# Performance work log

Measured on AMD Instinct MI355X. Metric: run time of the kernel, lower is better.

The kernel has to match this reference:

```python
import jax, jax.numpy as jnp
import numpy as np


def setup_inputs() -> dict:
    key = jax.random.key(0)
    k1, k2 = jax.random.split(key)
    pred = jax.random.normal(k1, (4, 8192, 3), dtype=jnp.float32)
    target = jax.random.normal(k2, (4, 8192, 3), dtype=jnp.float32)
    return {"pred": pred, "target": target}


def reference(pred, target):
    # Pairwise squared distances via the expansion ||p-q||^2 = ||p||^2 + ||q||^2 - 2 p.q
    # Avoids materializing the O(B*M*N*3) diff tensor of the naive broadcast.
    p_sq = jnp.sum(pred * pred, axis=-1)          # [B, M]
    q_sq = jnp.sum(target * target, axis=-1)      # [B, N]
    cross = jnp.einsum("bmd,bnd->bmn", pred, target)  # [B, M, N]
    dist_sq = p_sq[:, :, None] + q_sq[:, None, :] - 2.0 * cross  # [B, M, N]
    min_dist_pred = jnp.min(dist_sq, axis=2).mean(axis=1)    # [B] min over target per pred point
    min_dist_target = jnp.min(dist_sq, axis=1).mean(axis=1)  # [B] min over pred per target point
    return jnp.mean(min_dist_pred + min_dist_target)
```

## Files before the change

kernel.cpp:

```cpp
#include <hip/hip_runtime.h>


#define THREADS 256
#define P 8
#define S 16
#define G 128
#define TILE 128
#define LSTRIDE (TILE + 1)

__global__ __launch_bounds__(THREADS) void chamfer_min_kernel(
    const float* __restrict__ pred, const float* __restrict__ target,
    float* __restrict__ out, int M, float scale) {
  const int blocksPerDir = M / G;
  int pblk = blockIdx.x % blocksPerDir;
  int bd = blockIdx.x / blocksPerDir;
  int dir = bd & 1;
  int b = bd >> 1;
  const float* src = (dir ? target : pred) + (size_t)b * M * 3;
  const float* ref = (dir ? pred : target) + (size_t)b * M * 3;

  __shared__ float4 lds[S * LSTRIDE];

  int t = threadIdx.x;
  int g = t >> 4;
  int l = t & 15;

  float cm[P], ax[P], ay[P], az[P];
  int pbase = pblk * G;
#pragma unroll
  for (int j = 0; j < P; ++j) {
    int pt = pbase + l + 16 * j;
    float x = src[pt * 3 + 0], y = src[pt * 3 + 1], z = src[pt * 3 + 2];
    cm[j] = x * x + y * y + z * z;
    ax[j] = -2.f * x;
    ay[j] = -2.f * y;
    az[j] = -2.f * z;
  }
  float mins[P];
#pragma unroll
  for (int j = 0; j < P; ++j) mins[j] = 3.0e38f;

  const int sliceLen = M / S;
  const int ntiles = sliceLen / TILE;
  for (int k = 0; k < ntiles; ++k) {
    __syncthreads();
#pragma unroll
    for (int i = 0; i < (S * TILE) / THREADS; ++i) {
      int idx = t + THREADS * i;
      int s = idx >> 7;
      int jj = idx & (TILE - 1);
      int n = s * sliceLen + k * TILE + jj;
      float qx = ref[n * 3 + 0], qy = ref[n * 3 + 1], qz = ref[n * 3 + 2];
      lds[s * LSTRIDE + jj] = make_float4(qx, qy, qz, qx * qx + qy * qy + qz * qz);
    }
    __syncthreads();
    const float4* tp = lds + g * LSTRIDE;
#pragma unroll 2
    for (int j = 0; j < TILE; j += 4) {
      float4 q0 = tp[j + 0];
      float4 q1 = tp[j + 1];
      float4 q2 = tp[j + 2];
      float4 q3 = tp[j + 3];
#pragma unroll
      for (int p = 0; p < P; ++p) {
        float d0 = fmaf(ax[p], q0.x, fmaf(ay[p], q0.y, fmaf(az[p], q0.z, q0.w)));
        float d1 = fmaf(ax[p], q1.x, fmaf(ay[p], q1.y, fmaf(az[p], q1.z, q1.w)));
        float d2 = fmaf(ax[p], q2.x, fmaf(ay[p], q2.y, fmaf(az[p], q2.z, q2.w)));
        float d3 = fmaf(ax[p], q3.x, fmaf(ay[p], q3.y, fmaf(az[p], q3.z, q3.w)));
        mins[p] = fminf(fminf(mins[p], d0), d1);
        mins[p] = fminf(fminf(mins[p], d2), d3);
      }
    }
  }

  __syncthreads();
  float* lmin = (float*)lds;
  float* lcm = (float*)lds + S * G;
#pragma unroll
  for (int j = 0; j < P; ++j) {
    lmin[g * G + (l + 16 * j)] = mins[j];
    if (g == 0) lcm[l + 16 * j] = cm[j];
  }
  __syncthreads();
  float v = 0.f;
  if (t < G) {
    float mn = 3.0e38f;
#pragma unroll
    for (int s = 0; s < S; ++s) mn = fminf(mn, lmin[s * G + t]);
    v = lcm[t] + mn;
  }
  for (int off = 32; off > 0; off >>= 1) v += __shfl_down(v, off, 64);
  __shared__ float ws[THREADS / 64];
  if ((t & 63) == 0) ws[t >> 6] = v;
  __syncthreads();
  if (t == 0) {
    float bsum = 0.f;
#pragma unroll
    for (int w = 0; w < THREADS / 64; ++w) bsum += ws[w];
    atomicAdd(out, bsum * scale);
  }
}

extern "C" void kernel_launch(void* const* d_in, const int* in_sizes, int n_in,
                              void* d_out, int out_size, void* d_ws,
                              size_t ws_size, hipStream_t stream) {
  const float* pred = (const float*)d_in[0];
  const float* target = (const float*)d_in[1];
  float* out = (float*)d_out;
  const int B = 4;
  const int M = in_sizes[0] / (B * 3);

  float scale = 1.0f / (float)(B * M);

  hipMemsetAsync(out, 0, sizeof(float), stream);
  int blocks = B * 2 * (M / G);
  chamfer_min_kernel<<<blocks, THREADS, 0, stream>>>(pred, target, out, M,
                                                     scale);
}
```

Measured before the change: 97.13 us.

## Use packed FP32 FMA for distance math and double threads per block

The per-pair distance evaluation now uses v_pk_fma_f32 inline assembly, so each instruction computes two pred points against one reference point. This halves the FMA instruction count in the inner loop. The block also grows to 512 threads with 32 reference slices and 64-point tiles, and launch bounds request 4 blocks per CU. The tradeoff is pairing overhead from the packed operands and a larger LDS reduction buffer in the final min step.

```diff
diff --git a/kernel.cpp b/kernel.cpp
--- a/kernel.cpp
+++ b/kernel.cpp
@@ -1,14 +1,36 @@
 #include <hip/hip_runtime.h>
 
 
-#define THREADS 256
+#define THREADS 512
 #define P 8
-#define S 16
+#define S 32
 #define G 128
-#define TILE 128
+#define TILE 64
 #define LSTRIDE (TILE + 1)
 
-__global__ __launch_bounds__(THREADS) void chamfer_min_kernel(
+typedef float float2_t __attribute__((ext_vector_type(2)));
+typedef float float4_t __attribute__((ext_vector_type(4)));
+
+static __device__ __forceinline__ float2_t pk_fma_bl_bh(float2_t a, float2_t b) {
+  float2_t d;
+  asm("v_pk_fma_f32 %0, %1, %2, %2 op_sel:[0,0,1] op_sel_hi:[1,0,1]"
+      : "=v"(d) : "v"(a), "v"(b));
+  return d;
+}
+static __device__ __forceinline__ float2_t pk_fma_bh(float2_t a, float2_t b, float2_t c) {
+  float2_t d;
+  asm("v_pk_fma_f32 %0, %1, %2, %3 op_sel:[0,1,0] op_sel_hi:[1,1,1]"
+      : "=v"(d) : "v"(a), "v"(b), "v"(c));
+  return d;
+}
+static __device__ __forceinline__ float2_t pk_fma_bl(float2_t a, float2_t b, float2_t c) {
+  float2_t d;
+  asm("v_pk_fma_f32 %0, %1, %2, %3 op_sel:[0,0,0] op_sel_hi:[1,0,1]"
+      : "=v"(d) : "v"(a), "v"(b), "v"(c));
+  return d;
+}
+
+__global__ __launch_bounds__(THREADS, 4) void chamfer_min_kernel(
     const float* __restrict__ pred, const float* __restrict__ target,
     float* __restrict__ out, int M, float scale) {
   const int blocksPerDir = M / G;
@@ -19,26 +41,30 @@
   const float* src = (dir ? target : pred) + (size_t)b * M * 3;
   const float* ref = (dir ? pred : target) + (size_t)b * M * 3;
 
-  __shared__ float4 lds[S * LSTRIDE];
+  __shared__ float4_t lds[S * LSTRIDE];
 
   int t = threadIdx.x;
   int g = t >> 4;
   int l = t & 15;
 
-  float cm[P], ax[P], ay[P], az[P];
+  float cm[P];
+  float2_t a2x[P / 2], a2y[P / 2], a2z[P / 2];
   int pbase = pblk * G;
 #pragma unroll
-  for (int j = 0; j < P; ++j) {
-    int pt = pbase + l + 16 * j;
-    float x = src[pt * 3 + 0], y = src[pt * 3 + 1], z = src[pt * 3 + 2];
-    cm[j] = x * x + y * y + z * z;
-    ax[j] = -2.f * x;
-    ay[j] = -2.f * y;
-    az[j] = -2.f * z;
+  for (int i = 0; i < P / 2; ++i) {
+    int p0 = pbase + l + 16 * (2 * i);
+    int p1 = pbase + l + 16 * (2 * i + 1);
+    float x0 = src[p0 * 3 + 0], y0 = src[p0 * 3 + 1], z0 = src[p0 * 3 + 2];
+    float x1 = src[p1 * 3 + 0], y1 = src[p1 * 3 + 1], z1 = src[p1 * 3 + 2];
+    cm[2 * i] = x0 * x0 + y0 * y0 + z0 * z0;
+    cm[2 * i + 1] = x1 * x1 + y1 * y1 + z1 * z1;
+    a2x[i] = (float2_t){-2.f * x0, -2.f * x1};
+    a2y[i] = (float2_t){-2.f * y0, -2.f * y1};
+    a2z[i] = (float2_t){-2.f * z0, -2.f * z1};
   }
-  float mins[P];
+  float mlo[P / 2], mhi[P / 2];
 #pragma unroll
-  for (int j = 0; j < P; ++j) mins[j] = 3.0e38f;
+  for (int i = 0; i < P / 2; ++i) { mlo[i] = 3.0e38f; mhi[i] = 3.0e38f; }
 
   const int sliceLen = M / S;
   const int ntiles = sliceLen / TILE;
@@ -47,28 +73,43 @@
 #pragma unroll
     for (int i = 0; i < (S * TILE) / THREADS; ++i) {
       int idx = t + THREADS * i;
-      int s = idx >> 7;
+      int s = idx >> 6;
       int jj = idx & (TILE - 1);
       int n = s * sliceLen + k * TILE + jj;
       float qx = ref[n * 3 + 0], qy = ref[n * 3 + 1], qz = ref[n * 3 + 2];
-      lds[s * LSTRIDE + jj] = make_float4(qx, qy, qz, qx * qx + qy * qy + qz * qz);
+      lds[s * LSTRIDE + jj] =
+          (float4_t){qx, qy, qz, qx * qx + qy * qy + qz * qz};
     }
     __syncthreads();
-    const float4* tp = lds + g * LSTRIDE;
+    const float4_t* tp = lds + g * LSTRIDE;
 #pragma unroll 2
     for (int j = 0; j < TILE; j += 4) {
-      float4 q0 = tp[j + 0];
-      float4 q1 = tp[j + 1];
-      float4 q2 = tp[j + 2];
-      float4 q3 = tp[j + 3];
+      float4_t q0 = tp[j + 0];
+      float4_t q1 = tp[j + 1];
+      float4_t q2 = tp[j + 2];
+      float4_t q3 = tp[j + 3];
+      float2_t q0xy = __builtin_shufflevector(q0, q0, 0, 1);
+      float2_t q0zw = __builtin_shufflevector(q0, q0, 2, 3);
+      float2_t q1xy = __builtin_shufflevector(q1, q1, 0, 1);
+      float2_t q1zw = __builtin_shufflevector(q1, q1, 2, 3);
+      float2_t q2xy = __builtin_shufflevector(q2, q2, 0, 1);
+      float2_t q2zw = __builtin_shufflevector(q2, q2, 2, 3);
+      float2_t q3xy = __builtin_shufflevector(q3, q3, 0, 1);
+      float2_t q3zw = __builtin_shufflevector(q3, q3, 2, 3);
 #pragma unroll
-      for (int p = 0; p < P; ++p) {
-        float d0 = fmaf(ax[p], q0.x, fmaf(ay[p], q0.y, fmaf(az[p], q0.z, q0.w)));
-        float d1 = fmaf(ax[p], q1.x, fmaf(ay[p], q1.y, fmaf(az[p], q1.z, q1.w)));
-        float d2 = fmaf(ax[p], q2.x, fmaf(ay[p], q2.y, fmaf(az[p], q2.z, q2.w)));
-        float d3 = fmaf(ax[p], q3.x, fmaf(ay[p], q3.y, fmaf(az[p], q3.z, q3.w)));
-        mins[p] = fminf(fminf(mins[p], d0), d1);
-        mins[p] = fminf(fminf(mins[p], d2), d3);
+      for (int i = 0; i < P / 2; ++i) {
+        float2_t d0 = pk_fma_bl(a2x[i], q0xy,
+                        pk_fma_bh(a2y[i], q0xy, pk_fma_bl_bh(a2z[i], q0zw)));
+        float2_t d1 = pk_fma_bl(a2x[i], q1xy,
+                        pk_fma_bh(a2y[i], q1xy, pk_fma_bl_bh(a2z[i], q1zw)));
+        float2_t d2 = pk_fma_bl(a2x[i], q2xy,
+                        pk_fma_bh(a2y[i], q2xy, pk_fma_bl_bh(a2z[i], q2zw)));
+        float2_t d3 = pk_fma_bl(a2x[i], q3xy,
+                        pk_fma_bh(a2y[i], q3xy, pk_fma_bl_bh(a2z[i], q3zw)));
+        mlo[i] = fminf(fminf(mlo[i], d0.x), d1.x);
+        mlo[i] = fminf(fminf(mlo[i], d2.x), d3.x);
+        mhi[i] = fminf(fminf(mhi[i], d0.y), d1.y);
+        mhi[i] = fminf(fminf(mhi[i], d2.y), d3.y);
       }
     }
   }
@@ -77,9 +118,13 @@
   float* lmin = (float*)lds;
   float* lcm = (float*)lds + S * G;
 #pragma unroll
-  for (int j = 0; j < P; ++j) {
-    lmin[g * G + (l + 16 * j)] = mins[j];
-    if (g == 0) lcm[l + 16 * j] = cm[j];
+  for (int i = 0; i < P / 2; ++i) {
+    lmin[g * G + (l + 16 * (2 * i))] = mlo[i];
+    lmin[g * G + (l + 16 * (2 * i + 1))] = mhi[i];
+    if (g == 0) {
+      lcm[l + 16 * (2 * i)] = cm[2 * i];
+      lcm[l + 16 * (2 * i + 1)] = cm[2 * i + 1];
+    }
   }
   __syncthreads();
   float v = 0.f;
```

New measurement: 96.88 us. Within noise of the previous version (-0.3%).
